# Optimization experiments

Hardware: AMD Instinct MI355X
Metric: run time of the kernel (lower is better)

## Reference

```python
import jax, jax.numpy as jnp
import numpy as np


def setup_inputs() -> dict:
    key = jax.random.key(0)
    k1, k2, k3 = jax.random.split(key, 3)
    B, C, H, W, F, K = 8, 32, 64, 64, 64, 3
    x = jax.random.normal(k1, (B, C, H, W), dtype=jnp.float32)
    # per-weight rational (safe Pade [5/4]) coefficients: one activation per (f, a, b, c)
    num_coef = jax.random.normal(k2, (F, K, K, C, 6), dtype=jnp.float32) * 0.1
    den_coef = jax.random.normal(k3, (F, K, K, C, 4), dtype=jnp.float32) * 0.1
    return {"x": x, "num_coef": num_coef, "den_coef": den_coef}


def _rational(x, an, bd):
    """Safe Pade rational: P(x)/(1+|x*(b1+x*(b2+x*(b3+x*b4)))|).
    x: [B,H,W,K,K,C]; an: [K,K,C,6]; bd: [K,K,C,4] (broadcast over B,H,W)."""
    num = an[..., 5]
    for i in (4, 3, 2, 1, 0):  # Horner, ascending coeff order a0..a5
        num = num * x + an[..., i]
    q = bd[..., 3]
    for i in (2, 1, 0):
        q = q * x + bd[..., i]
    den = 1.0 + jnp.abs(q * x)
    return num / den


def reference(x, num_coef, den_coef):
    B, C, H, W = x.shape
    F, K = num_coef.shape[0], num_coef.shape[1]
    p = (K - 1) // 2
    xp = jnp.pad(x, ((0, 0), (0, 0), (p, p), (p, p)))  # zero pad H,W
    xp = jnp.transpose(xp, (0, 2, 3, 1))  # [B, H+2p, W+2p, C]
    # im2col patches: [B, H, W, K, K, C]
    patches = jnp.stack(
        [jnp.stack([xp[:, a:a + H, b:b + W, :] for b in range(K)], axis=3)
         for a in range(K)], axis=3)

    def per_filter(coefs):
        an, bd = coefs  # [K,K,C,6], [K,K,C,4]
        y = _rational(patches, an, bd)  # [B,H,W,K,K,C]
        return jnp.sum(y, axis=(3, 4, 5))  # [B,H,W]

    out = jax.lax.map(per_filter, (num_coef, den_coef))  # [F,B,H,W]
    return jnp.transpose(out, (1, 0, 2, 3))  # [B,F,H,W]
```

## Files before the change

### kernel.cpp

```cpp
#include <hip/hip_runtime.h>


typedef int   iv4  __attribute__((ext_vector_type(4)));
typedef short s8v  __attribute__((ext_vector_type(8)));
typedef float f16v __attribute__((ext_vector_type(16)));

#define Bb 8
#define Cc 32
#define Hh 64
#define Ww 64
#define Ff 64
#define PW 66
#define PPLANE (PW * PW)
#define NELEM  (Bb * Cc * PPLANE)
#define NTAP   288
#define PWBLK  (NELEM / 256)

static __device__ __forceinline__ unsigned short f2bf(float f) {
    unsigned u = __builtin_bit_cast(unsigned, f);
    u += 0x7fffu + ((u >> 16) & 1u);
    return (unsigned short)(u >> 16);
}
static __device__ __forceinline__ float bf2f(unsigned short h) {
    unsigned u = ((unsigned)h) << 16;
    return __builtin_bit_cast(float, u);
}
static __device__ __forceinline__ int pack2(unsigned short a, unsigned short b) {
    return (int)((unsigned)a | ((unsigned)b << 16));
}

__global__ __launch_bounds__(256) void prep_kernel(
    const float* __restrict__ x,
    const float* __restrict__ ncf, const float* __restrict__ dcf,
    iv4* __restrict__ pw, iv4* __restrict__ ac)
{
    if ((int)blockIdx.x < PWBLK) {
        int idx = (int)blockIdx.x * 256 + (int)threadIdx.x;
        int wp = idx % PW;
        int r1 = idx / PW;
        int hp = r1 % PW;
        int pl = r1 / PW;
        float v = 0.0f;
        if (hp >= 1 && hp <= Hh && wp >= 1 && wp <= Ww)
            v = x[((size_t)pl * Hh + (hp - 1)) * Ww + (wp - 1)];
        float p2 = v * v, p3 = p2 * v, p4 = p2 * p2, p5 = p4 * v;
        float pv[6] = {1.0f, v, p2, p3, p4, p5};
        unsigned short hi[6], lo[6];
#pragma unroll
        for (int e = 0; e < 6; ++e) {
            hi[e] = f2bf(pv[e]);
            lo[e] = f2bf(pv[e] - bf2f(hi[e]));
        }
        iv4 r0, r1v;
        r0.x  = pack2(hi[0], hi[1]); r0.y  = pack2(hi[2], hi[3]);
        r0.z  = pack2(hi[4], hi[5]); r0.w  = pack2(lo[1], lo[2]);
        r1v.x = pack2(lo[3], lo[4]); r1v.y = pack2(lo[5], hi[1]);
        r1v.z = pack2(hi[2], hi[3]); r1v.w = pack2(hi[4], hi[5]);
        pw[idx]         = r0;
        pw[NELEM + idx] = r1v;
    } else {
        int idx = ((int)blockIdx.x - PWBLK) * 256 + (int)threadIdx.x;
        int l = idx & 63, tile = (idx >> 6) & 3, t = idx >> 8;
        int m = l & 31, g = l >> 5;
        float cv[6];
        if (tile < 2) {
            int f = tile * 32 + m;
            const float* s = ncf + ((size_t)f * NTAP + t) * 6;
            cv[0] = s[0]; cv[1] = s[1]; cv[2] = s[2];
            cv[3] = s[3]; cv[4] = s[4]; cv[5] = s[5];
        } else {
            int f = (tile - 2) * 32 + m;
            const float* s = dcf + ((size_t)f * NTAP + t) * 4;
            cv[0] = 0.0f; cv[1] = s[0]; cv[2] = s[1];
            cv[3] = s[2]; cv[4] = s[3]; cv[5] = 0.0f;
        }
        unsigned short chi[6], clo[6];
#pragma unroll
        for (int e = 0; e < 6; ++e) {
            chi[e] = f2bf(cv[e]);
            clo[e] = f2bf(cv[e] - bf2f(chi[e]));
        }
        iv4 o;
        if (g == 0) {
            o.x = pack2(chi[0], chi[1]); o.y = pack2(chi[2], chi[3]);
            o.z = pack2(chi[4], chi[5]); o.w = pack2(chi[1], chi[2]);
        } else {
            o.x = pack2(chi[3], chi[4]); o.y = pack2(chi[5], clo[1]);
            o.z = pack2(clo[2], clo[3]); o.w = pack2(clo[4], clo[5]);
        }
        ac[idx] = o;
    }
}

__global__ __launch_bounds__(512, 4) void kan_mfma_kernel(
    const iv4* __restrict__ pw, const iv4* __restrict__ ac,
    float* __restrict__ out)
{
    const int tid = threadIdx.x;
    const int l = tid & 63, v = tid >> 6, ln = l & 31, g = l >> 5;
    const int p = v & 1, q = v >> 1;
    const int gb = (int)blockIdx.x;
    const int wh = gb & 1, h = (gb >> 1) & 63, bb = gb >> 7;
    const int w0 = wh << 5;

    __shared__ float red[4][2][64][16];

    f16v acc, zf;
#pragma unroll
    for (int r = 0; r < 16; ++r) { acc[r] = 0.0f; zf[r] = 0.0f; }

    const iv4* __restrict__ pwg = pw + (size_t)g * NELEM;
    const int t0 = q * 72;

    {
    }
    int k20 = t0 >> 5;
    int dy0 = k20 / 3, dx0 = k20 - 3 * dy0;
    int elemBase = ((bb * Cc + (t0 & 31)) * PW + (h + dy0)) * PW + (w0 + ln + dx0);
    const iv4* apl = ac + (size_t)t0 * 256 + p * 64 + l;

#pragma unroll 1
    for (int j = 0; j < 36; ++j) {
        const int tp = t0 + 2 * j;
        if (j > 0) {
            if ((tp & 31) == 0) {
                const int k2 = tp >> 5;
                const int dy = k2 / 3, dx = k2 - 3 * dy;
                elemBase = (bb * Cc * PW + (h + dy)) * PW + (w0 + ln + dx);
            } else {
                elemBase += 2 * PPLANE;
            }
        }

        iv4 B0  = pwg[elemBase];
        iv4 B1  = pwg[elemBase + PPLANE];
        iv4 An0 = apl[0],   Ad0 = apl[128];
        iv4 An1 = apl[256], Ad1 = apl[384];
        apl += 512;

        s8v b0 = __builtin_bit_cast(s8v, B0);
        s8v b1 = __builtin_bit_cast(s8v, B1);

        f16v Dn0 = __builtin_amdgcn_mfma_f32_32x32x16_bf16(
            __builtin_bit_cast(s8v, An0), b0, zf, 0, 0, 0);
        f16v Dd0 = __builtin_amdgcn_mfma_f32_32x32x16_bf16(
            __builtin_bit_cast(s8v, Ad0), b0, zf, 0, 0, 0);
        f16v Dn1 = __builtin_amdgcn_mfma_f32_32x32x16_bf16(
            __builtin_bit_cast(s8v, An1), b1, zf, 0, 0, 0);
        f16v Dd1 = __builtin_amdgcn_mfma_f32_32x32x16_bf16(
            __builtin_bit_cast(s8v, Ad1), b1, zf, 0, 0, 0);

#pragma unroll
        for (int r = 0; r < 16; ++r) {
            float da = 1.0f + __builtin_fabsf(Dd0[r]);
            float db = 1.0f + __builtin_fabsf(Dd1[r]);
            float nn = __builtin_fmaf(Dn0[r], db, Dn1[r] * da);
            float rc = __builtin_amdgcn_rcpf(da * db);
            acc[r] = __builtin_fmaf(nn, rc, acc[r]);
        }
    }

#pragma unroll
    for (int r = 0; r < 16; ++r)
        red[q][p][l][r ^ ((l >> 1) & 15)] = acc[r];
    __syncthreads();

    const int p2 = v & 1;
#pragma unroll
    for (int jj = 0; jj < 4; ++jj) {
        int r = (v >> 1) * 4 + jj;
        int rs = r ^ ((l >> 1) & 15);
        float s = red[0][p2][l][rs] + red[1][p2][l][rs]
                + red[2][p2][l][rs] + red[3][p2][l][rs];
        int f = p2 * 32 + (r & 3) + ((r >> 2) << 3) + ((l >> 5) << 2);
        out[(((size_t)bb * Ff + f) * Hh + h) * Ww + w0 + ln] = s;
    }
}

extern "C" void kernel_launch(void* const* d_in, const int* in_sizes, int n_in,
                              void* d_out, int out_size, void* d_ws, size_t ws_size,
                              hipStream_t stream) {
    const float* x   = (const float*)d_in[0];
    const float* ncf = (const float*)d_in[1];
    const float* dcf = (const float*)d_in[2];
    float* out = (float*)d_out;

    iv4* pw = (iv4*)d_ws;
    iv4* ac = pw + 2 * NELEM;

    prep_kernel<<<PWBLK + NTAP, 256, 0, stream>>>(x, ncf, dcf, pw, ac);
    kan_mfma_kernel<<<1024, 512, 0, stream>>>(pw, ac, out);
}
```

Measured before the change: 163.9 us.

## Switch to 16x16x32 MFMA tiles with per-wave filter groups, drop LDS reduction

Replaces the 32x32x16 MFMA formulation with 16x16x32 bf16 MFMAs, where each wave owns 16 filters and 16 pixels and loops over all 288 taps. This removes the cross-wave shared-memory reduction and the __syncthreads. Blocks shrink to 256 threads, and the grid doubles to 2048 with higher occupancy bounds. The coefficient layout is re-packed for the new fragment shape, and a zero element in the workspace pads unused K lanes. In exchange, each wave does more serial iterations, and the fragment loads are smaller and more numerous.

```diff
diff --git a/kernel.cpp b/kernel.cpp
--- a/kernel.cpp
+++ b/kernel.cpp
@@ -1,9 +1,9 @@
 #include <hip/hip_runtime.h>
 
 
-typedef int   iv4  __attribute__((ext_vector_type(4)));
-typedef short s8v  __attribute__((ext_vector_type(8)));
-typedef float f16v __attribute__((ext_vector_type(16)));
+typedef int   iv4 __attribute__((ext_vector_type(4)));
+typedef short s8v __attribute__((ext_vector_type(8)));
+typedef float f4v __attribute__((ext_vector_type(4)));
 
 #define Bb 8
 #define Cc 32
@@ -14,7 +14,11 @@
 #define PPLANE (PW * PW)
 #define NELEM  (Bb * Cc * PPLANE)
 #define NTAP   288
+#define NTP    144
 #define PWBLK  (NELEM / 256)
+#define ACTN   (NTP * 4 * 4 * 64)
+#define ABLK   (ACTN / 256)
+#define ZIDX   (2 * NELEM)
 
 static __device__ __forceinline__ unsigned short f2bf(float f) {
     unsigned u = __builtin_bit_cast(unsigned, f);
@@ -28,14 +32,18 @@
 static __device__ __forceinline__ int pack2(unsigned short a, unsigned short b) {
     return (int)((unsigned)a | ((unsigned)b << 16));
 }
+static __device__ __forceinline__ iv4 ld16(const char* p) {
+    return *(const iv4* __restrict__)p;
+}
 
 __global__ __launch_bounds__(256) void prep_kernel(
     const float* __restrict__ x,
     const float* __restrict__ ncf, const float* __restrict__ dcf,
-    iv4* __restrict__ pw, iv4* __restrict__ ac)
+    iv4* __restrict__ pw)
 {
     if ((int)blockIdx.x < PWBLK) {
         int idx = (int)blockIdx.x * 256 + (int)threadIdx.x;
+        if (idx == 0) { iv4 z = {0, 0, 0, 0}; pw[ZIDX] = z; }
         int wp = idx % PW;
         int r1 = idx / PW;
         int hp = r1 % PW;
@@ -60,16 +68,20 @@
         pw[NELEM + idx] = r1v;
     } else {
         int idx = ((int)blockIdx.x - PWBLK) * 256 + (int)threadIdx.x;
-        int l = idx & 63, tile = (idx >> 6) & 3, t = idx >> 8;
-        int m = l & 31, g = l >> 5;
+        int l  = idx & 63;
+        int j  = (idx >> 6) & 3;
+        int fg = (idx >> 8) & 3;
+        int tp = idx >> 10;
+        int t  = 2 * tp + (j >> 1);
+        int nd = j & 1;
+        int f  = fg * 16 + (l & 15);
+        int half = (l >> 4) & 1;
         float cv[6];
-        if (tile < 2) {
-            int f = tile * 32 + m;
+        if (nd == 0) {
             const float* s = ncf + ((size_t)f * NTAP + t) * 6;
             cv[0] = s[0]; cv[1] = s[1]; cv[2] = s[2];
             cv[3] = s[3]; cv[4] = s[4]; cv[5] = s[5];
         } else {
-            int f = (tile - 2) * 32 + m;
             const float* s = dcf + ((size_t)f * NTAP + t) * 4;
             cv[0] = 0.0f; cv[1] = s[0]; cv[2] = s[1];
             cv[3] = s[2]; cv[4] = s[3]; cv[5] = 0.0f;
@@ -81,100 +93,89 @@
             clo[e] = f2bf(cv[e] - bf2f(chi[e]));
         }
         iv4 o;
-        if (g == 0) {
+        if (half == 0) {
             o.x = pack2(chi[0], chi[1]); o.y = pack2(chi[2], chi[3]);
             o.z = pack2(chi[4], chi[5]); o.w = pack2(chi[1], chi[2]);
         } else {
             o.x = pack2(chi[3], chi[4]); o.y = pack2(chi[5], clo[1]);
             o.z = pack2(clo[2], clo[3]); o.w = pack2(clo[4], clo[5]);
         }
-        ac[idx] = o;
+        iv4* act = pw + (ZIDX + 1);
+        act[idx] = o;
     }
 }
 
-__global__ __launch_bounds__(512, 4) void kan_mfma_kernel(
-    const iv4* __restrict__ pw, const iv4* __restrict__ ac,
-    float* __restrict__ out)
+__global__ __launch_bounds__(256, 8) void kan_mfma_kernel(
+    const iv4* __restrict__ pw, float* __restrict__ out)
 {
     const int tid = threadIdx.x;
-    const int l = tid & 63, v = tid >> 6, ln = l & 31, g = l >> 5;
-    const int p = v & 1, q = v >> 1;
+    const int l  = tid & 63, fg = tid >> 6;
+    const int px = l & 15, g = l >> 4;
     const int gb = (int)blockIdx.x;
-    const int wh = gb & 1, h = (gb >> 1) & 63, bb = gb >> 7;
-    const int w0 = wh << 5;
+    const int wq = gb & 3, h = (gb >> 2) & 63, bb = gb >> 8;
+    const int w0 = wq << 4;
 
-    __shared__ float red[4][2][64][16];
+    const char* __restrict__ pwc  = (const char*)pw;
+    const char* __restrict__ actc = (const char*)(pw + (ZIDX + 1));
 
-    f16v acc, zf;
-#pragma unroll
-    for (int r = 0; r < 16; ++r) { acc[r] = 0.0f; zf[r] = 0.0f; }
+    const unsigned laneBaseB =
+        (g == 0) ? (unsigned)(px * 16)
+      : (g == 1) ? (unsigned)((NELEM + px) * 16)
+      :            (unsigned)(ZIDX * 16);
+    const unsigned maskE = (g < 2) ? 0xFFFFFFFFu : 0u;
+    const unsigned dB    = ((unsigned)(PPLANE * 16)) & maskE;
 
-    const iv4* __restrict__ pwg = pw + (size_t)g * NELEM;
-    const int t0 = q * 72;
+    f4v acc = {0.0f, 0.0f, 0.0f, 0.0f};
+    f4v zf  = {0.0f, 0.0f, 0.0f, 0.0f};
 
-    {
-    }
-    int k20 = t0 >> 5;
-    int dy0 = k20 / 3, dx0 = k20 - 3 * dy0;
-    int elemBase = ((bb * Cc + (t0 & 31)) * PW + (h + dy0)) * PW + (w0 + ln + dx0);
-    const iv4* apl = ac + (size_t)t0 * 256 + p * 64 + l;
+    unsigned offA = (unsigned)(fg * 4096 + l * 16);
 
 #pragma unroll 1
-    for (int j = 0; j < 36; ++j) {
-        const int tp = t0 + 2 * j;
-        if (j > 0) {
-            if ((tp & 31) == 0) {
-                const int k2 = tp >> 5;
-                const int dy = k2 / 3, dx = k2 - 3 * dy;
-                elemBase = (bb * Cc * PW + (h + dy)) * PW + (w0 + ln + dx);
-            } else {
-                elemBase += 2 * PPLANE;
-            }
-        }
+    for (int k2 = 0; k2 < 9; ++k2) {
+        const int dy = k2 / 3, dx = k2 - 3 * dy;
+        const int elemw = ((bb * Cc) * PW + (h + dy)) * PW + (w0 + dx);
+        unsigned offB = laneBaseB + (((unsigned)(elemw * 16)) & maskE);
 
-        iv4 B0  = pwg[elemBase];
-        iv4 B1  = pwg[elemBase + PPLANE];
-        iv4 An0 = apl[0],   Ad0 = apl[128];
-        iv4 An1 = apl[256], Ad1 = apl[384];
-        apl += 512;
+#pragma unroll 1
+        for (int pp = 0; pp < 16; ++pp) {
+            iv4 B0 = ld16(pwc + offB);
+            unsigned offB1 = offB + dB;
+            iv4 B1 = ld16(pwc + offB1);
+            offB = offB1 + dB;
 
-        s8v b0 = __builtin_bit_cast(s8v, B0);
-        s8v b1 = __builtin_bit_cast(s8v, B1);
+            iv4 An0 = ld16(actc + offA);
+            iv4 Ad0 = ld16(actc + offA + 1024);
+            iv4 An1 = ld16(actc + offA + 2048);
+            iv4 Ad1 = ld16(actc + offA + 3072);
+            offA += 16384;
 
-        f16v Dn0 = __builtin_amdgcn_mfma_f32_32x32x16_bf16(
-            __builtin_bit_cast(s8v, An0), b0, zf, 0, 0, 0);
-        f16v Dd0 = __builtin_amdgcn_mfma_f32_32x32x16_bf16(
-            __builtin_bit_cast(s8v, Ad0), b0, zf, 0, 0, 0);
-        f16v Dn1 = __builtin_amdgcn_mfma_f32_32x32x16_bf16(
-            __builtin_bit_cast(s8v, An1), b1, zf, 0, 0, 0);
-        f16v Dd1 = __builtin_amdgcn_mfma_f32_32x32x16_bf16(
-            __builtin_bit_cast(s8v, Ad1), b1, zf, 0, 0, 0);
+            s8v b0 = __builtin_bit_cast(s8v, B0);
+            s8v b1 = __builtin_bit_cast(s8v, B1);
+
+            f4v Dn0 = __builtin_amdgcn_mfma_f32_16x16x32_bf16(
+                __builtin_bit_cast(s8v, An0), b0, zf, 0, 0, 0);
+            f4v Dd0 = __builtin_amdgcn_mfma_f32_16x16x32_bf16(
+                __builtin_bit_cast(s8v, Ad0), b0, zf, 0, 0, 0);
+            f4v Dn1 = __builtin_amdgcn_mfma_f32_16x16x32_bf16(
+                __builtin_bit_cast(s8v, An1), b1, zf, 0, 0, 0);
+            f4v Dd1 = __builtin_amdgcn_mfma_f32_16x16x32_bf16(
+                __builtin_bit_cast(s8v, Ad1), b1, zf, 0, 0, 0);
 
 #pragma unroll
-        for (int r = 0; r < 16; ++r) {
-            float da = 1.0f + __builtin_fabsf(Dd0[r]);
-            float db = 1.0f + __builtin_fabsf(Dd1[r]);
-            float nn = __builtin_fmaf(Dn0[r], db, Dn1[r] * da);
-            float rc = __builtin_amdgcn_rcpf(da * db);
-            acc[r] = __builtin_fmaf(nn, rc, acc[r]);
+            for (int r = 0; r < 4; ++r) {
+                float da = 1.0f + __builtin_fabsf(Dd0[r]);
+                float db = 1.0f + __builtin_fabsf(Dd1[r]);
+                float nn = __builtin_fmaf(Dn0[r], db, Dn1[r] * da);
+                float rc = __builtin_amdgcn_rcpf(da * db);
+                acc[r] = __builtin_fmaf(nn, rc, acc[r]);
+            }
         }
     }
 
+    float* o = out + (((size_t)(bb * Ff + fg * 16 + g * 4) * Hh + h) * Ww) + w0 + px;
 #pragma unroll
-    for (int r = 0; r < 16; ++r)
-        red[q][p][l][r ^ ((l >> 1) & 15)] = acc[r];
-    __syncthreads();
-
-    const int p2 = v & 1;
-#pragma unroll
-    for (int jj = 0; jj < 4; ++jj) {
-        int r = (v >> 1) * 4 + jj;
-        int rs = r ^ ((l >> 1) & 15);
-        float s = red[0][p2][l][rs] + red[1][p2][l][rs]
-                + red[2][p2][l][rs] + red[3][p2][l][rs];
-        int f = p2 * 32 + (r & 3) + ((r >> 2) << 3) + ((l >> 5) << 2);
-        out[(((size_t)bb * Ff + f) * Hh + h) * Ww + w0 + ln] = s;
-    }
+    for (int r = 0; r < 4; ++r)
+        o[(size_t)r * Hh * Ww] = acc[r];
 }
 
 extern "C" void kernel_launch(void* const* d_in, const int* in_sizes, int n_in,
@@ -186,8 +187,7 @@
     float* out = (float*)d_out;
 
     iv4* pw = (iv4*)d_ws;
-    iv4* ac = pw + 2 * NELEM;
 
-    prep_kernel<<<PWBLK + NTAP, 256, 0, stream>>>(x, ncf, dcf, pw, ac);
-    kan_mfma_kernel<<<1024, 512, 0, stream>>>(pw, ac, out);
+    prep_kernel<<<PWBLK + ABLK, 256, 0, stream>>>(x, ncf, dcf, pw);
+    kan_mfma_kernel<<<2048, 256, 0, stream>>>(pw, out);
 }
```

After: 315.0 us. 1.92x slower.
